# Performance work log

Hardware: AMD Instinct MI355X
Metric: run time of the kernel (lower is better)

The kernel has to match this reference:

```python
import jax, jax.numpy as jnp
import numpy as np

EMBED = 1024
HEADS = 16
HEAD_DIM = EMBED // HEADS
B, S = 2, 2048


def setup_inputs() -> dict:
    key = jax.random.key(0)
    ks = jax.random.split(key, 11)
    sc = 1.0 / np.sqrt(EMBED)
    d = {
        'query': jax.random.normal(ks[0], (B, S, EMBED), jnp.float32),
        'key':   jax.random.normal(ks[1], (B, S, EMBED), jnp.float32),
        'value': jax.random.normal(ks[2], (B, S, EMBED), jnp.float32),
        'Wq': jax.random.normal(ks[3], (EMBED, EMBED), jnp.float32) * sc,
        'bq': jnp.zeros((EMBED,), jnp.float32),
        'Wk': jax.random.normal(ks[4], (EMBED, EMBED), jnp.float32) * sc,
        'bk': jnp.zeros((EMBED,), jnp.float32),
        'Wv': jax.random.normal(ks[5], (EMBED, EMBED), jnp.float32) * sc,
        'bv': jnp.zeros((EMBED,), jnp.float32),
        'Wo': jax.random.normal(ks[6], (EMBED, EMBED), jnp.float32) * sc,
        'bo': jnp.zeros((EMBED,), jnp.float32),
    }
    return d


def _split_heads(x):
    b, s, _ = x.shape
    return x.reshape(b, s, HEADS, HEAD_DIM).transpose(0, 2, 1, 3)  # [B,H,S,D]


def reference(query, key, value, Wq, bq, Wk, bk, Wv, bv, Wo, bo):
    # nn.Linear: y = x @ W^T + b
    q = _split_heads(query @ Wq.T + bq)
    k = _split_heads(key @ Wk.T + bk)
    v = _split_heads(value @ Wv.T + bv)
    scale = 1.0 / np.sqrt(HEAD_DIM).astype(np.float32)
    attn = jnp.einsum('bhqd,bhkd->bhqk', q, k) * scale  # [B,H,S,S]
    attn = jax.nn.softmax(attn, axis=-1)
    out = jnp.einsum('bhqk,bhkd->bhqd', attn, v)
    out = out.transpose(0, 2, 1, 3).reshape(query.shape[0], -1, EMBED)
    return out @ Wo.T + bo
```

## Files before the change

### kernel.cpp

```cpp
#include <hip/hip_runtime.h>

typedef _Float16 f16;
typedef __fp16   fp16n2 __attribute__((ext_vector_type(2)));
typedef _Float16 f16x8 __attribute__((ext_vector_type(8)));
typedef float    f32x2 __attribute__((ext_vector_type(2)));
typedef float    f32x4 __attribute__((ext_vector_type(4)));
typedef float    f32x16 __attribute__((ext_vector_type(16)));
typedef int      i32x2 __attribute__((ext_vector_type(2)));
typedef unsigned short u16;
typedef unsigned long long u64;

#define B_ 2
#define S_ 2048
#define E_ 1024
#define H_ 16
#define D_ 64
#define M_ (B_*S_)
#define LOG2E 1.44269504088896340736f

__device__ __forceinline__ f32x4 mfma16(f16x8 a, f16x8 b, f32x4 c) {
  return __builtin_amdgcn_mfma_f32_16x16x32_f16(a, b, c, 0, 0, 0);
}
__device__ __forceinline__ f32x16 mfma32(f16x8 a, f16x8 b, f32x16 c) {
  return __builtin_amdgcn_mfma_f32_32x32x16_f16(a, b, c, 0, 0, 0);
}

__device__ __forceinline__ void gload_lds16(const void* g, void* l) {
  __builtin_amdgcn_global_load_lds(
      (const __attribute__((address_space(1))) unsigned int*)g,
      (__attribute__((address_space(3))) unsigned int*)l, 16, 0, 0);
}

__device__ __forceinline__ int pkrtz(float a, float b) {
  union { fp16n2 h; int i; } u;
  u.h = __builtin_amdgcn_cvt_pkrtz(a, b);
  return u.i;
}

__device__ __forceinline__ u16 f16bits(float x) {
  union { f16 h; u16 u; } c; c.h = (f16)x; return c.u;
}

__device__ __forceinline__ f32x16 Z16() {
  f32x16 z = {0.f,0.f,0.f,0.f,0.f,0.f,0.f,0.f,0.f,0.f,0.f,0.f,0.f,0.f,0.f,0.f};
  return z;
}

__device__ __forceinline__ f32x2 pr2(const f32x16& v, int j) {
  return (f32x2){v[2 * j], v[2 * j + 1]};
}

__global__ __launch_bounds__(256) void cast_all(
    const float* __restrict__ q, const float* __restrict__ k, const float* __restrict__ v,
    const float* __restrict__ wq, const float* __restrict__ wk,
    const float* __restrict__ wv, const float* __restrict__ wo,
    f16* __restrict__ xq, f16* __restrict__ xk, f16* __restrict__ xv,
    f16* __restrict__ wqh, f16* __restrict__ wkh, f16* __restrict__ wvh,
    f16* __restrict__ woh) {
  int i = blockIdx.x * 256 + threadIdx.x;
  const float* src; f16* dst; int off;
  if (i < 3 * 524288) {
    int seg = i >> 19; off = i & 524287;
    src = seg == 0 ? q : seg == 1 ? k : v;
    dst = seg == 0 ? xq : seg == 1 ? xk : xv;
  } else {
    int j = i - 3 * 524288;
    int seg = j >> 17; off = j & 131071;
    src = seg == 0 ? wq : seg == 1 ? wk : seg == 2 ? wv : wo;
    dst = seg == 0 ? wqh : seg == 1 ? wkh : seg == 2 ? wvh : woh;
  }
  const float4* s = (const float4*)src;
  float4 a = s[off * 2], b = s[off * 2 + 1];
  f16x8 o = { (f16)a.x, (f16)a.y, (f16)a.z, (f16)a.w,
              (f16)b.x, (f16)b.y, (f16)b.z, (f16)b.w };
  *(f16x8*)&dst[(size_t)off * 8] = o;
}

__device__ __forceinline__ void gemm_core64(const f16* __restrict__ A,
                                            const f16* __restrict__ Bm,
                                            int m0, int n0,
                                            f32x4 (&acc)[4][2]) {
  __shared__ f16 Al[2][128 * 32];
  __shared__ f16 Bl[2][64 * 32];
  const int tid = threadIdx.x;
  const int w = tid >> 6, lane = tid & 63, lg = lane >> 4, ll = lane & 15;
  const int wr = (w >> 1) * 64, wc = (w & 1) * 32;

  const f32x4 zero4 = {0.f, 0.f, 0.f, 0.f};
#pragma unroll
  for (int m = 0; m < 4; ++m) { acc[m][0] = zero4; acc[m][1] = zero4; }

  const int lgs = (lg ^ ((ll >> 1) & 3)) * 8;

  for (int k0 = 0; k0 < 1024; k0 += 64) {
    __syncthreads();
#pragma unroll
    for (int ks = 0; ks < 2; ++ks) {
#pragma unroll
      for (int it = 0; it < 2; ++it) {
        int chunk = it * 256 + tid;
        int row = chunk >> 2;
        int c8 = ((chunk & 3) ^ ((chunk >> 3) & 3)) * 8;
        gload_lds16(&A[(size_t)(m0 + row) * 1024 + k0 + ks * 32 + c8],
                    &Al[ks][chunk * 8]);
      }
      {
        int chunk = tid;
        int row = chunk >> 2;
        int c8 = ((chunk & 3) ^ ((chunk >> 3) & 3)) * 8;
        gload_lds16(&Bm[(size_t)(n0 + row) * 1024 + k0 + ks * 32 + c8],
                    &Bl[ks][chunk * 8]);
      }
    }
    __syncthreads();

#pragma unroll
    for (int ks = 0; ks < 2; ++ks) {
      f16x8 af[4], bf[2];
#pragma unroll
      for (int m = 0; m < 4; ++m) af[m] = *(const f16x8*)&Al[ks][(wr + m * 16 + ll) * 32 + lgs];
#pragma unroll
      for (int n = 0; n < 2; ++n) bf[n] = *(const f16x8*)&Bl[ks][(wc + n * 16 + ll) * 32 + lgs];
#pragma unroll
      for (int m = 0; m < 4; ++m)
#pragma unroll
        for (int n = 0; n < 2; ++n) acc[m][n] = mfma16(af[m], bf[n], acc[m][n]);
    }
  }
}

__global__ __launch_bounds__(256) void gemm_qkv(
    const f16* __restrict__ Xq, const f16* __restrict__ Xk, const f16* __restrict__ Xv,
    const f16* __restrict__ Wq, const f16* __restrict__ Wk, const f16* __restrict__ Wv,
    const float* __restrict__ bq, const float* __restrict__ bk, const float* __restrict__ bv,
    f16* __restrict__ Qb, f16* __restrict__ Kb, f16* __restrict__ Vt) {
  const int z = blockIdx.z;
  const f16*   A    = (z == 0) ? Xq : (z == 1) ? Xk : Xv;
  const f16*   Bm   = (z == 0) ? Wq : (z == 1) ? Wk : Wv;
  const float* bias = (z == 0) ? bq : (z == 1) ? bk : bv;
  const float scale = (z == 0) ? (0.125f * LOG2E) : 1.0f;
  const int m0 = blockIdx.x * 128, n0 = blockIdx.y * 64;

  f32x4 acc[4][2];
  gemm_core64(A, Bm, m0, n0, acc);

  const int tid = threadIdx.x;
  const int w = tid >> 6, lane = tid & 63, lg = lane >> 4, ll = lane & 15;
  const int wr = (w >> 1) * 64, wc = (w & 1) * 32;

  if (z == 2) {
#pragma unroll
    for (int m = 0; m < 4; ++m)
#pragma unroll
      for (int n = 0; n < 2; ++n) {
        int col = n0 + wc + n * 16 + ll;
        float bv_ = bias[col];
        int h = col >> 6, d = col & 63;
        int rowb = m0 + wr + m * 16 + lg * 4;
        int b = rowb >> 11, s = rowb & 2047;
        u64 pk = (u64)f16bits(acc[m][n][0] + bv_)
               | ((u64)f16bits(acc[m][n][1] + bv_) << 16)
               | ((u64)f16bits(acc[m][n][2] + bv_) << 32)
               | ((u64)f16bits(acc[m][n][3] + bv_) << 48);
        *(u64*)&Vt[(((size_t)(b * H_ + h)) * D_ + d) * S_ + s] = pk;
      }
    return;
  }

  f16* dst = (z == 0) ? Qb : Kb;
#pragma unroll
  for (int m = 0; m < 4; ++m)
#pragma unroll
    for (int n = 0; n < 2; ++n) {
      int col = n0 + wc + n * 16 + ll;
      float bv_ = bias[col];
      int h = col >> 6, d = col & 63;
#pragma unroll
      for (int r = 0; r < 4; ++r) {
        int row = m0 + wr + m * 16 + lg * 4 + r;
        int b = row >> 11, s = row & 2047;
        float v = (acc[m][n][r] + bv_) * scale;
        dst[(((size_t)(b * H_ + h)) * S_ + s) * D_ + d] = (f16)v;
      }
    }
}

__global__ __launch_bounds__(256) void gemm_out(const f16* __restrict__ A,
                                                const f16* __restrict__ W,
                                                const float* __restrict__ bias,
                                                float* __restrict__ out) {
  const int m0 = blockIdx.x * 128, n0 = blockIdx.y * 64;
  f32x4 acc[4][2];
  gemm_core64(A, W, m0, n0, acc);

  const int tid = threadIdx.x;
  const int w = tid >> 6, lane = tid & 63, lg = lane >> 4, ll = lane & 15;
  const int wr = (w >> 1) * 64, wc = (w & 1) * 32;
#pragma unroll
  for (int m = 0; m < 4; ++m)
#pragma unroll
    for (int n = 0; n < 2; ++n) {
      int col = n0 + wc + n * 16 + ll;
      float bv_ = bias[col];
#pragma unroll
      for (int r = 0; r < 4; ++r) {
        int row = m0 + wr + m * 16 + lg * 4 + r;
        out[(size_t)row * 1024 + col] = acc[m][n][r] + bv_;
      }
    }
}

__global__ __launch_bounds__(512, 4) void attn_fwd(const f16* __restrict__ Q,
                                                   const f16* __restrict__ K,
                                                   const f16* __restrict__ VT,
                                                   f16* __restrict__ O) {
  const int qt = blockIdx.x, bh = blockIdx.y;
  const int tid = threadIdx.x;
  const int w = tid >> 6, lane = tid & 63;
  const int ql = lane & 31, hi = lane >> 5;
  const int qsub = w & 3, kvh = w >> 2;

  __shared__ __align__(16) char smem[65536];
  char* hbase = smem + kvh * 32768;

  const f16* Qb = Q  + (size_t)bh * S_ * D_;
  const f16* Kb = K  + (size_t)bh * S_ * D_ + (size_t)(kvh * 1024) * D_;
  const f16* Vb = VT + (size_t)bh * D_ * S_ + kvh * 1024;
  const int q0 = qt * 128 + qsub * 32;

  f16x8 qf[4];
#pragma unroll
  for (int ks = 0; ks < 4; ++ks)
    qf[ks] = *(const f16x8*)&Qb[(size_t)(q0 + ql) * 64 + ks * 16 + hi * 8];

  f32x16 accO[2];
  accO[0] = Z16(); accO[1] = Z16();
  float l_r = 0.f;

  const int seg = w & 3;
  const int lr = lane >> 3;
  const int lc = lane & 7;
  const int cs = lc ^ lr;

#define STAGE(kt_)                                                             \
  {                                                                            \
    char* Kl_ = hbase + ((kt_) & 1) * 16384;                                   \
    char* Vl_ = Kl_ + 8192;                                                    \
    _Pragma("unroll")                                                          \
    for (int i_ = 0; i_ < 2; ++i_) {                                           \
      int r_ = seg * 16 + i_ * 8 + lr;                                         \
      gload_lds16(&Kb[(size_t)((kt_) * 64 + r_) * 64 + cs * 8],                \
                  Kl_ + seg * 2048 + i_ * 1024);                               \
      gload_lds16(&Vb[(size_t)r_ * S_ + (kt_) * 64 + cs * 8],                  \
                  Vl_ + seg * 2048 + i_ * 1024);                               \
    }                                                                          \
  }

  STAGE(0);

#pragma unroll 1
  for (int kt = 0; kt < 16; ++kt) {
    __syncthreads();
    if (kt + 1 < 16) STAGE(kt + 1);

    char* KlB = hbase + (kt & 1) * 16384;
    char* VlB = KlB + 8192;

    f32x16 accS[2];
    __builtin_amdgcn_s_setprio(1);
#pragma unroll
    for (int c = 0; c < 2; ++c) {
      int row = c * 32 + ql;
      int rb = row * 128, sw = (row & 7) << 4;
      f16x8 kf0 = *(const f16x8*)(KlB + rb + ((hi * 16) ^ sw));
      accS[c] = mfma32(kf0, qf[0], Z16());
#pragma unroll
      for (int ks = 1; ks < 4; ++ks) {
        f16x8 kf = *(const f16x8*)(KlB + rb + (((ks * 2 + hi) * 16) ^ sw));
        accS[c] = mfma32(kf, qf[ks], accS[c]);
      }
    }
    __builtin_amdgcn_s_setprio(0);

    f32x2 rs2 = {0.f, 0.f};
#pragma unroll
    for (int c = 0; c < 2; ++c)
#pragma unroll
      for (int j = 0; j < 8; ++j) {
        float p0 = __builtin_amdgcn_exp2f(accS[c][2 * j]);
        float p1 = __builtin_amdgcn_exp2f(accS[c][2 * j + 1]);
        accS[c][2 * j]     = p0;
        accS[c][2 * j + 1] = p1;
        rs2 += (f32x2){p0, p1};
      }
    l_r += rs2.x + rs2.y;

#pragma unroll
    for (int c = 0; c < 2; ++c)
#pragma unroll
      for (int s = 0; s < 2; ++s) {
        int b0 = s * 8;
        int a0 = pkrtz(accS[c][b0 + 0], accS[c][b0 + 1]);
        int a1 = pkrtz(accS[c][b0 + 2], accS[c][b0 + 3]);
        int a2 = pkrtz(accS[c][b0 + 4], accS[c][b0 + 5]);
        int a3 = pkrtz(accS[c][b0 + 6], accS[c][b0 + 7]);
        i32x2 r02 = __builtin_amdgcn_permlane32_swap(a0, a2, false, false);
        i32x2 r13 = __builtin_amdgcn_permlane32_swap(a1, a3, false, false);
        union { int i[4]; f16x8 h; } pf;
        pf.i[0] = r02.x; pf.i[1] = r13.x; pf.i[2] = r02.y; pf.i[3] = r13.y;
        int kvb = c * 64 + s * 32 + hi * 16;
        __builtin_amdgcn_s_setprio(1);
#pragma unroll
        for (int dc = 0; dc < 2; ++dc) {
          int dr = dc * 32 + ql;
          f16x8 vf = *(const f16x8*)(VlB + dr * 128 + (kvb ^ ((dr & 7) << 4)));
          accO[dc] = mfma32(vf, pf.h, accO[dc]);
        }
        __builtin_amdgcn_s_setprio(0);
      }
  }
#undef STAGE

  l_r += __shfl_xor(l_r, 32);

  __syncthreads();
  float* lB = (float*)smem;
  if (kvh == 1) {
    if (hi == 0) lB[qsub * 32 + ql] = l_r;
#pragma unroll
    for (int dc = 0; dc < 2; ++dc)
#pragma unroll
      for (int g = 0; g < 4; ++g) {
        int d0 = g * 8 + hi * 4 + dc * 32;
        f32x4 v = { accO[dc][g * 4 + 0], accO[dc][g * 4 + 1],
                    accO[dc][g * 4 + 2], accO[dc][g * 4 + 3] };
        *(f32x4*)(smem + 32768 + qsub * 8192 + ql * 256 + ((d0 * 4) ^ ((ql & 7) << 4))) = v;
      }
  }
  __syncthreads();
  f16* Ep = (f16*)(smem + 1024);
  if (kvh == 0) {
    float inv = 1.0f / (l_r + lB[qsub * 32 + ql]);
#pragma unroll
    for (int dc = 0; dc < 2; ++dc)
#pragma unroll
      for (int g = 0; g < 4; ++g) {
        int d0 = g * 8 + hi * 4 + dc * 32;
        f32x4 o2 = *(const f32x4*)(smem + 32768 + qsub * 8192 + ql * 256 +
                                   ((d0 * 4) ^ ((ql & 7) << 4)));
        u64 pk = (u64)f16bits((accO[dc][g * 4 + 0] + o2[0]) * inv)
               | ((u64)f16bits((accO[dc][g * 4 + 1] + o2[1]) * inv) << 16)
               | ((u64)f16bits((accO[dc][g * 4 + 2] + o2[2]) * inv) << 32)
               | ((u64)f16bits((accO[dc][g * 4 + 3] + o2[3]) * inv) << 48);
        *(u64*)&Ep[(qsub * 32 + ql) * 68 + d0] = pk;
      }
  }
  __syncthreads();
  const int b = bh >> 4, h = bh & 15;
#pragma unroll
  for (int pass = 0; pass < 2; ++pass) {
    int idx = pass * 512 + tid;
    int row = idx >> 3, cx = idx & 7;
    f16x8 v = *(const f16x8*)&Ep[row * 68 + cx * 8];
    *(f16x8*)&O[((size_t)(b * S_ + qt * 128 + row)) * E_ + h * 64 + cx * 8] = v;
  }
}

extern "C" void kernel_launch(void* const* d_in, const int* in_sizes, int n_in,
                              void* d_out, int out_size, void* d_ws, size_t ws_size,
                              hipStream_t stream) {
  (void)in_sizes; (void)n_in; (void)out_size; (void)ws_size;
  const float* q  = (const float*)d_in[0];
  const float* k  = (const float*)d_in[1];
  const float* v  = (const float*)d_in[2];
  const float* Wq = (const float*)d_in[3];
  const float* bq = (const float*)d_in[4];
  const float* Wk = (const float*)d_in[5];
  const float* bk = (const float*)d_in[6];
  const float* Wv = (const float*)d_in[7];
  const float* bv = (const float*)d_in[8];
  const float* Wo = (const float*)d_in[9];
  const float* bo = (const float*)d_in[10];
  float* out = (float*)d_out;

  f16* ws  = (f16*)d_ws;
  f16* Xq  = ws;
  f16* Xk  = Xq  + (size_t)M_ * E_;
  f16* Xv  = Xk  + (size_t)M_ * E_;
  f16* Wqh = Xv  + (size_t)M_ * E_;
  f16* Wkh = Wqh + (size_t)E_ * E_;
  f16* Wvh = Wkh + (size_t)E_ * E_;
  f16* Woh = Wvh + (size_t)E_ * E_;
  f16* Qb  = Woh + (size_t)E_ * E_;
  f16* Kb  = Qb  + (size_t)M_ * E_;
  f16* VTb = Kb  + (size_t)M_ * E_;
  f16* AO  = Xq;

  cast_all<<<8192, 256, 0, stream>>>(q, k, v, Wq, Wk, Wv, Wo,
                                     Xq, Xk, Xv, Wqh, Wkh, Wvh, Woh);

  gemm_qkv<<<dim3(M_ / 128, E_ / 64, 3), 256, 0, stream>>>(
      Xq, Xk, Xv, Wqh, Wkh, Wvh, bq, bk, bv, Qb, Kb, VTb);

  attn_fwd<<<dim3(S_ / 128, B_ * H_), 512, 0, stream>>>(Qb, Kb, VTb, AO);

  gemm_out<<<dim3(M_ / 128, E_ / 64), 256, 0, stream>>>(AO, Woh, bo, out);
}
```

Baseline: 118.8 us.

## Read V fragments directly from global memory and halve attention LDS footprint

The attention kernel no longer stages V^T tiles into shared memory. Each wave now loads its V fragments straight from global memory inside the PV loop, which halves the LDS allocation from 64KB to 32KB and is meant to allow more resident blocks per CU. The cross-half reduction of the output accumulator is also exchanged through LDS in fp16 instead of fp32 so it fits the smaller buffer. In exchange, V loads become uncoalesced strided global reads on the critical MFMA path with no prefetch, and the partial sums lose some precision.

```diff
diff --git a/kernel.cpp b/kernel.cpp
--- a/kernel.cpp
+++ b/kernel.cpp
@@ -220,12 +220,12 @@
   const int ql = lane & 31, hi = lane >> 5;
   const int qsub = w & 3, kvh = w >> 2;
 
-  __shared__ __align__(16) char smem[65536];
-  char* hbase = smem + kvh * 32768;
+  __shared__ __align__(16) char smem[32768];
+  char* hbase = smem + kvh * 16384;
 
   const f16* Qb = Q  + (size_t)bh * S_ * D_;
   const f16* Kb = K  + (size_t)bh * S_ * D_ + (size_t)(kvh * 1024) * D_;
-  const f16* Vb = VT + (size_t)bh * D_ * S_ + kvh * 1024;
+  const f16* Vg = VT + (size_t)bh * D_ * S_ + kvh * 1024;
   const int q0 = qt * 128 + qsub * 32;
 
   f16x8 qf[4];
@@ -244,15 +244,12 @@
 
 #define STAGE(kt_)                                                             \
   {                                                                            \
-    char* Kl_ = hbase + ((kt_) & 1) * 16384;                                   \
-    char* Vl_ = Kl_ + 8192;                                                    \
+    char* Kl_ = hbase + ((kt_) & 1) * 8192;                                    \
     _Pragma("unroll")                                                          \
     for (int i_ = 0; i_ < 2; ++i_) {                                           \
       int r_ = seg * 16 + i_ * 8 + lr;                                         \
       gload_lds16(&Kb[(size_t)((kt_) * 64 + r_) * 64 + cs * 8],                \
                   Kl_ + seg * 2048 + i_ * 1024);                               \
-      gload_lds16(&Vb[(size_t)r_ * S_ + (kt_) * 64 + cs * 8],                  \
-                  Vl_ + seg * 2048 + i_ * 1024);                               \
     }                                                                          \
   }
 
@@ -263,8 +260,7 @@
     __syncthreads();
     if (kt + 1 < 16) STAGE(kt + 1);
 
-    char* KlB = hbase + (kt & 1) * 16384;
-    char* VlB = KlB + 8192;
+    char* KlB = hbase + (kt & 1) * 8192;
 
     f32x16 accS[2];
     __builtin_amdgcn_s_setprio(1);
@@ -308,12 +304,12 @@
         i32x2 r13 = __builtin_amdgcn_permlane32_swap(a1, a3, false, false);
         union { int i[4]; f16x8 h; } pf;
         pf.i[0] = r02.x; pf.i[1] = r13.x; pf.i[2] = r02.y; pf.i[3] = r13.y;
-        int kvb = c * 64 + s * 32 + hi * 16;
+        int kve = c * 32 + s * 16 + hi * 8;
         __builtin_amdgcn_s_setprio(1);
 #pragma unroll
         for (int dc = 0; dc < 2; ++dc) {
           int dr = dc * 32 + ql;
-          f16x8 vf = *(const f16x8*)(VlB + dr * 128 + (kvb ^ ((dr & 7) << 4)));
+          f16x8 vf = *(const f16x8*)&Vg[(size_t)dr * S_ + kt * 64 + kve];
           accO[dc] = mfma32(vf, pf.h, accO[dc]);
         }
         __builtin_amdgcn_s_setprio(0);
@@ -325,6 +321,7 @@
 
   __syncthreads();
   float* lB = (float*)smem;
+  f16* Ep = (f16*)(smem + 1024);
   if (kvh == 1) {
     if (hi == 0) lB[qsub * 32 + ql] = l_r;
 #pragma unroll
@@ -332,13 +329,14 @@
 #pragma unroll
       for (int g = 0; g < 4; ++g) {
         int d0 = g * 8 + hi * 4 + dc * 32;
-        f32x4 v = { accO[dc][g * 4 + 0], accO[dc][g * 4 + 1],
-                    accO[dc][g * 4 + 2], accO[dc][g * 4 + 3] };
-        *(f32x4*)(smem + 32768 + qsub * 8192 + ql * 256 + ((d0 * 4) ^ ((ql & 7) << 4))) = v;
+        u64 pk = (u64)f16bits(accO[dc][g * 4 + 0])
+               | ((u64)f16bits(accO[dc][g * 4 + 1]) << 16)
+               | ((u64)f16bits(accO[dc][g * 4 + 2]) << 32)
+               | ((u64)f16bits(accO[dc][g * 4 + 3]) << 48);
+        *(u64*)&Ep[(qsub * 32 + ql) * 68 + d0] = pk;
       }
   }
   __syncthreads();
-  f16* Ep = (f16*)(smem + 1024);
   if (kvh == 0) {
     float inv = 1.0f / (l_r + lB[qsub * 32 + ql]);
 #pragma unroll
@@ -346,12 +344,12 @@
 #pragma unroll
       for (int g = 0; g < 4; ++g) {
         int d0 = g * 8 + hi * 4 + dc * 32;
-        f32x4 o2 = *(const f32x4*)(smem + 32768 + qsub * 8192 + ql * 256 +
-                                   ((d0 * 4) ^ ((ql & 7) << 4)));
-        u64 pk = (u64)f16bits((accO[dc][g * 4 + 0] + o2[0]) * inv)
-               | ((u64)f16bits((accO[dc][g * 4 + 1] + o2[1]) * inv) << 16)
-               | ((u64)f16bits((accO[dc][g * 4 + 2] + o2[2]) * inv) << 32)
-               | ((u64)f16bits((accO[dc][g * 4 + 3] + o2[3]) * inv) << 48);
+        union { u64 v; f16 h[4]; } o2;
+        o2.v = *(const u64*)&Ep[(qsub * 32 + ql) * 68 + d0];
+        u64 pk = (u64)f16bits((accO[dc][g * 4 + 0] + (float)o2.h[0]) * inv)
+               | ((u64)f16bits((accO[dc][g * 4 + 1] + (float)o2.h[1]) * inv) << 16)
+               | ((u64)f16bits((accO[dc][g * 4 + 2] + (float)o2.h[2]) * inv) << 32)
+               | ((u64)f16bits((accO[dc][g * 4 + 3] + (float)o2.h[3]) * inv) << 48);
         *(u64*)&Ep[(qsub * 32 + ql) * 68 + d0] = pk;
       }
   }
```

Result: slower. 144.4 us (+21.5%).
